# Optimization experiments

Measured on AMD Instinct MI355X. Metric: run time of the kernel, lower is better.

Reference implementation:

```python
import jax, jax.numpy as jnp
import numpy as np

B, T, E, H, V = 64, 160, 512, 1024, 32000


def setup_inputs() -> dict:
    key = jax.random.key(0)
    ks = jax.random.split(key, 8)
    s = 1.0 / np.sqrt(H).astype(np.float32)
    return {
        "contexts": jax.random.randint(ks[0], (B, T), 0, V),
        "responses": jax.random.randint(ks[1], (B, T), 0, V),
        "emb": jax.random.normal(ks[2], (V, E), jnp.float32) * 0.02,
        "Wih": jax.random.uniform(ks[3], (4 * H, E), jnp.float32, -s, s),
        "Whh": jax.random.uniform(ks[4], (4 * H, H), jnp.float32, -s, s),
        "bih": jax.random.uniform(ks[5], (4 * H,), jnp.float32, -s, s),
        "bhh": jax.random.uniform(ks[6], (4 * H,), jnp.float32, -s, s),
        "M": jax.random.normal(ks[7], (H, H), jnp.float32),
    }


def _lstm_final_h(tokens, emb, Wih, Whh, bih, bhh):
    """Single-layer LSTM (PyTorch gate order i,f,g,o); returns final hidden state [B,H]."""
    x = emb[tokens]                      # [B, T, E]
    b = bih + bhh                        # [4H]
    hdim = Whh.shape[1]

    def step(carry, xt):
        h, c = carry
        gates = xt @ Wih.T + h @ Whh.T + b          # [B, 4H]
        i, f, g, o = jnp.split(gates, 4, axis=-1)
        c = jax.nn.sigmoid(f) * c + jax.nn.sigmoid(i) * jnp.tanh(g)
        h = jax.nn.sigmoid(o) * jnp.tanh(c)
        return (h, c), None

    h0 = jnp.zeros((tokens.shape[0], hdim), x.dtype)
    (h, _), _ = jax.lax.scan(step, (h0, h0), jnp.swapaxes(x, 0, 1))  # scan over time
    return h


def reference(contexts, responses, emb, Wih, Whh, bih, bhh, M):
    ch = _lstm_final_h(contexts, emb, Wih, Whh, bih, bhh)   # [B, H]
    rh = _lstm_final_h(responses, emb, Wih, Whh, bih, bhh)  # [B, H]
    # batched bilinear: sigmoid(diag(C @ M @ R^T)) -- replaces the per-example Python loop
    return jax.nn.sigmoid(jnp.einsum('bi,ij,bj->b', ch, M, rh))
```

## Files before the change

kernel.cpp:

```cpp
#include <hip/hip_runtime.h>
#include <math.h>


#define BB 64
#define TT 160
#define EE 512
#define HH 1024
#define G4 4096
#define ROWS 128
#define NBLK 64

typedef unsigned short u16;
typedef unsigned int u32;
typedef __attribute__((ext_vector_type(8))) __bf16 bf16x8;
typedef __attribute__((ext_vector_type(8))) short short8;
typedef __attribute__((ext_vector_type(4))) short short4v;
typedef __attribute__((ext_vector_type(4))) float f32x4;
typedef __attribute__((ext_vector_type(2))) u32 u32x2;

__device__ __forceinline__ u16 f2b(float f) {
    unsigned u = __float_as_uint(f);
    u = u + 0x7fffu + ((u >> 16) & 1u);
    return (u16)(u >> 16);
}
__device__ __forceinline__ float b2f(u16 s) { return __uint_as_float(((unsigned)s) << 16); }

#define LOG2E 1.4426950408889634f
__device__ __forceinline__ float sigf(float x) {
    return __builtin_amdgcn_rcpf(1.f + __builtin_amdgcn_exp2f(-LOG2E * x));
}
__device__ __forceinline__ float tanhf_fast(float x) {
    return 1.f - 2.f * __builtin_amdgcn_rcpf(1.f + __builtin_amdgcn_exp2f(2.f * LOG2E * x));
}

__device__ __forceinline__ f32x4 mfma16(short8 a, short8 b, f32x4 c) {
    return __builtin_amdgcn_mfma_f32_16x16x32_bf16(
        __builtin_bit_cast(bf16x8, a), __builtin_bit_cast(bf16x8, b), c, 0, 0, 0);
}

__device__ __forceinline__ void g2l16(const void* gsrc, void* ldst) {
    __builtin_amdgcn_global_load_lds(
        (const __attribute__((address_space(1))) u32*)gsrc,
        (__attribute__((address_space(3))) u32*)ldst, 16, 0, 0);
}
__device__ __forceinline__ void g2l16c(const void* gsrc, void* ldst) {
    __builtin_amdgcn_global_load_lds(
        (const __attribute__((address_space(1))) u32*)gsrc,
        (__attribute__((address_space(3))) u32*)ldst, 16, 0, 17);
}

__global__ __launch_bounds__(256) void cvt_kernel(const float* __restrict__ in,
                                                  u16* __restrict__ out, int n4) {
    int i = blockIdx.x * 256 + threadIdx.x;
    if (i < n4) {
        f32x4 v = *(const f32x4*)(in + (size_t)i * 4);
        short4v o;
        o.x = (short)f2b(v.x); o.y = (short)f2b(v.y);
        o.z = (short)f2b(v.z); o.w = (short)f2b(v.w);
        *(short4v*)(out + (size_t)i * 4) = o;
    }
}

__global__ __launch_bounds__(256) void pre_gemm2(
    const int* __restrict__ ctx, const int* __restrict__ rsp,
    const u16* __restrict__ embb, const u16* __restrict__ Wihb,
    const float* __restrict__ bih, const float* __restrict__ bhh,
    u16* __restrict__ xg)
{
    __shared__ __align__(16) u16 As[2][128][64];
    __shared__ __align__(16) u16 Ws[2][128][64];
    __shared__ int toks[128];
    const int tid = threadIdx.x;
    const int n0 = blockIdx.x * 128;
    const int t  = blockIdx.y;

    if (tid < 128) {
        int r = tid;
        toks[tid] = (r < BB) ? ctx[r * TT + t] : rsp[(r - BB) * TT + t];
    }
    __syncthreads();

    const u16* asrc[4]; const u16* bsrc[4];
    #pragma unroll
    for (int q = 0; q < 4; ++q) {
        int i = tid + q * 256;
        int row = i >> 3, c16 = i & 7;
        int scol = ((c16 ^ (row & 7)) * 8);
        asrc[q] = embb + (size_t)toks[row] * EE + scol;
        bsrc[q] = Wihb + (size_t)(n0 + row) * EE + scol;
    }

    const int lane = tid & 63, wave = tid >> 6;
    const int wr = (wave >> 1) * 64, wc = (wave & 1) * 64;
    const int l15 = lane & 15, l4 = lane >> 4;
    f32x4 acc[4][4] = {};

    #pragma unroll
    for (int q = 0; q < 4; ++q) {
        g2l16(asrc[q], (char*)&As[0][0][0] + (tid + q * 256) * 16);
        g2l16(bsrc[q], (char*)&Ws[0][0][0] + (tid + q * 256) * 16);
    }
    for (int it = 0; it < 8; ++it) {
        __syncthreads();
        if (it + 1 < 8) {
            int kk = (it + 1) * 64, bs = (it + 1) & 1;
            #pragma unroll
            for (int q = 0; q < 4; ++q) {
                g2l16(asrc[q] + kk, (char*)&As[bs][0][0] + (tid + q * 256) * 16);
                g2l16(bsrc[q] + kk, (char*)&Ws[bs][0][0] + (tid + q * 256) * 16);
            }
        }
        const int b = it & 1;
        #pragma unroll
        for (int ks = 0; ks < 2; ++ks) {
            int c16 = ks * 4 + l4;
            short8 a[4], w[4];
            #pragma unroll
            for (int mf = 0; mf < 4; ++mf) {
                int R = wr + mf * 16 + l15;
                a[mf] = *(const short8*)((const char*)&As[b][0][0] + R * 128 + ((c16 ^ (R & 7)) << 4));
            }
            #pragma unroll
            for (int nf = 0; nf < 4; ++nf) {
                int Nn = wc + nf * 16 + l15;
                w[nf] = *(const short8*)((const char*)&Ws[b][0][0] + Nn * 128 + ((c16 ^ (Nn & 7)) << 4));
            }
            #pragma unroll
            for (int mf = 0; mf < 4; ++mf)
                #pragma unroll
                for (int nf = 0; nf < 4; ++nf)
                    acc[mf][nf] = mfma16(a[mf], w[nf], acc[mf][nf]);
        }
    }

    u16* xp = xg + (size_t)t * ROWS * G4;
    #pragma unroll
    for (int nf = 0; nf < 4; ++nf) {
        int n = n0 + wc + nf * 16 + l15;
        float bias = bih[n] + bhh[n];
        #pragma unroll
        for (int mf = 0; mf < 4; ++mf)
            #pragma unroll
            for (int q = 0; q < 4; ++q) {
                int r = wr + mf * 16 + l4 * 4 + q;
                xp[(size_t)r * G4 + n] = f2b(acc[mf][nf][q] + bias);
            }
    }
}

__global__ __launch_bounds__(512, 2) void lstm_persist7(
    const u16* __restrict__ Whhb, const u16* __restrict__ xg,
    u16* __restrict__ hbuf, u32* __restrict__ barr)
{
    __shared__ __align__(16) u16 Abuf[2][64][512];

    const int tid = threadIdx.x;
    const int bx = blockIdx.x;
    const int cg = bx & 31, rg = bx >> 5;
    const int r0 = rg * 64, j0 = cg * 32;
    const int lane = tid & 63, w = tid >> 6;
    const int colt = w >> 2, q = w & 3;
    const int l15 = lane & 15, l4 = lane >> 4;

    float* const G = (float*)&Abuf[0][0][0];

    short8 breg[4][8];
    #pragma unroll
    for (int nt = 0; nt < 4; ++nt) {
        int n = (colt * 2 + (nt >> 1)) * 1024 + j0 + (nt & 1) * 16 + l15;
        const u16* wp = Whhb + (size_t)n * HH + l4 * 8;
        #pragma unroll
        for (int z = 0; z < 8; ++z) {
            int kc = (z < 4) ? (q * 4 + z) : (16 + q * 4 + (z - 4));
            breg[nt][z] = *(const short8*)(wp + kc * 32);
        }
    }

    const int urow = tid >> 3;
    const int jj4  = (tid & 7) * 4;
    float cst[4] = {0.f, 0.f, 0.f, 0.f};

    u32* const cb = barr + (size_t)rg * 2048;

    __syncthreads();

    for (int t = 0; t < TT; ++t) {
        const u16* hin = hbuf + (size_t)(t & 1) * ROWS * HH;
        u16* hout      = hbuf + (size_t)((t + 1) & 1) * ROWS * HH;

        #pragma unroll
        for (int j = 0; j < 8; ++j) {
            int row = w * 8 + j;
            const u16* src = hin + (size_t)(r0 + row) * HH + ((lane ^ (row & 7)) * 8);
            g2l16c(src,       &Abuf[0][row][0]);
            g2l16c(src + 512, &Abuf[1][row][0]);
        }
        u32x2 xv[4];
        {
            const u16* xp = xg + ((size_t)t * ROWS + r0 + urow) * G4 + j0 + jj4;
            #pragma unroll
            for (int g = 0; g < 4; ++g)
                asm volatile("global_load_dwordx2 %0, %1, off"
                             : "=v"(xv[g]) : "v"(xp + g * HH));
        }

        f32x4 acc[4][4] = {};

        asm volatile("s_waitcnt vmcnt(4)" ::: "memory");
        __builtin_amdgcn_sched_barrier(0);
        __builtin_amdgcn_s_barrier();
        __builtin_amdgcn_sched_barrier(0);
        #pragma unroll
        for (int half = 0; half < 2; ++half) {
            #pragma unroll
            for (int z4 = 0; z4 < 4; ++z4) {
                const int kcl = q * 4 + z4;
                short8 a[4];
                #pragma unroll
                for (int rt = 0; rt < 4; ++rt) {
                    int row = rt * 16 + l15;
                    int c16 = kcl * 4 + l4;
                    a[rt] = *(const short8*)((const char*)&Abuf[half][0][0] +
                             row * 1024 + ((c16 ^ (l15 & 7)) << 4));
                }
                #pragma unroll
                for (int rt = 0; rt < 4; ++rt)
                    #pragma unroll
                    for (int nt = 0; nt < 4; ++nt)
                        acc[rt][nt] = mfma16(a[rt], breg[nt][half * 4 + z4], acc[rt][nt]);
            }
        }
        asm volatile("s_waitcnt lgkmcnt(0)" ::: "memory");
        __builtin_amdgcn_s_barrier();
        __builtin_amdgcn_sched_barrier(0);

        if (q < 2) {
            #pragma unroll
            for (int rt = 0; rt < 4; ++rt)
                #pragma unroll
                for (int nt = 0; nt < 4; ++nt) {
                    int col = colt * 64 + nt * 16 + l15;
                    int rowb = rt * 16 + l4 * 4;
                    #pragma unroll
                    for (int e = 0; e < 4; ++e)
                        G[((size_t)q * 64 + rowb + e) * 132 + col] = acc[rt][nt][e];
                }
        }
        asm volatile("s_waitcnt lgkmcnt(0)" ::: "memory");
        __builtin_amdgcn_s_barrier();
        __builtin_amdgcn_sched_barrier(0);
        if (q >= 2) {
            #pragma unroll
            for (int rt = 0; rt < 4; ++rt)
                #pragma unroll
                for (int nt = 0; nt < 4; ++nt) {
                    int col = colt * 64 + nt * 16 + l15;
                    int rowb = rt * 16 + l4 * 4;
                    #pragma unroll
                    for (int e = 0; e < 4; ++e)
                        G[((size_t)(q - 2) * 64 + rowb + e) * 132 + col] += acc[rt][nt][e];
                }
        }
        asm volatile("s_waitcnt lgkmcnt(0)" ::: "memory");
        __builtin_amdgcn_s_barrier();
        __builtin_amdgcn_sched_barrier(0);

        asm volatile("s_waitcnt vmcnt(0)" ::: "memory");
        float gv[4][4];
        #pragma unroll
        for (int g = 0; g < 4; ++g) {
            const float* Gr0 = &G[((size_t)0 * 64 + urow) * 132 + g * 32 + jj4];
            const float* Gr1 = &G[((size_t)1 * 64 + urow) * 132 + g * 32 + jj4];
            f32x4 a0 = *(const f32x4*)Gr0;
            f32x4 a1 = *(const f32x4*)Gr1;
            gv[g][0] = a0.x + a1.x + b2f((u16)(xv[g].x & 0xffffu));
            gv[g][1] = a0.y + a1.y + b2f((u16)(xv[g].x >> 16));
            gv[g][2] = a0.z + a1.z + b2f((u16)(xv[g].y & 0xffffu));
            gv[g][3] = a0.w + a1.w + b2f((u16)(xv[g].y >> 16));
        }
        u16 hp[4];
        #pragma unroll
        for (int e = 0; e < 4; ++e) {
            float ii = sigf(gv[0][e]);
            float ff = sigf(gv[1][e]);
            float gg = tanhf_fast(gv[2][e]);
            float oo = sigf(gv[3][e]);
            cst[e] = ff * cst[e] + ii * gg;
            hp[e] = f2b(oo * tanhf_fast(cst[e]));
        }
        u32x2 hw;
        hw.x = (u32)hp[0] | ((u32)hp[1] << 16);
        hw.y = (u32)hp[2] | ((u32)hp[3] << 16);
        {
            u16* hpt = hout + (size_t)(r0 + urow) * HH + j0 + jj4;
            asm volatile("global_store_dwordx2 %0, %1, off sc0 sc1"
                         :: "v"(hpt), "v"(hw) : "memory");
        }

        if (t < TT - 1) {
            asm volatile("s_waitcnt vmcnt(0)" ::: "memory");
            __builtin_amdgcn_s_barrier();
            __builtin_amdgcn_sched_barrier(0);
            const u32 target = (u32)(t + 1);
            if (tid == 0)
                asm volatile("global_store_dword %0, %1, off sc0 sc1"
                             :: "v"(cb + cg * 32), "v"(target) : "memory");
            if (w == 0) {
                const u32* fp = cb + (lane & 31) * 32;
                int spins = 0;
                while (true) {
                    u32 v;
                    asm volatile("global_load_dword %0, %1, off sc0 sc1"
                                 : "=v"(v) : "v"(fp));
                    asm volatile("s_waitcnt vmcnt(0)" ::: "memory");
                    if (__all(v >= target)) break;
                    __builtin_amdgcn_s_sleep(1);
                    if (++spins > 2000000) break;
                }
            }
            __builtin_amdgcn_s_barrier();
            __builtin_amdgcn_sched_barrier(0);
        }
    }
}

template<int MODE>
__global__ __launch_bounds__(256) void step_fused(
    const int* __restrict__ ctx, const int* __restrict__ rsp,
    const u16* __restrict__ embb, const u16* __restrict__ Wihb,
    const u16* __restrict__ Whhb, const u16* __restrict__ xg,
    const float* __restrict__ bih, const float* __restrict__ bhh,
    const u16* __restrict__ hin, u16* __restrict__ hout,
    float* __restrict__ c_ws, int t)
{
    __shared__ __align__(16) u16 As[2][64][64];
    __shared__ __align__(16) u16 Ws[2][32][64];
    __shared__ float gs[64][32];
    __shared__ int toks[64];

    const int tid = threadIdx.x;
    const int cg = blockIdx.x & 127, rg = blockIdx.x >> 7;
    const int r0 = rg * 64, j0 = cg * 8;

    if (MODE == 1) {
        if (tid < 64) {
            int r = r0 + tid;
            toks[tid] = (r < BB) ? ctx[r * TT + t] : rsp[(r - BB) * TT + t];
        }
        __syncthreads();
    }

    const int arow0 = tid >> 3, c16a = tid & 7;
    const int arow1 = arow0 + 32;
    const int acol0 = ((c16a ^ (arow0 & 7)) * 8);
    const int acol1 = ((c16a ^ (arow1 & 7)) * 8);
    const u16* hA0 = hin + (size_t)(r0 + arow0) * HH + acol0;
    const u16* hA1 = hin + (size_t)(r0 + arow1) * HH + acol1;
    const u16* eA0 = nullptr; const u16* eA1 = nullptr;
    if (MODE == 1) {
        eA0 = embb + (size_t)toks[arow0] * EE + acol0;
        eA1 = embb + (size_t)toks[arow1] * EE + acol1;
    }
    const int nn = tid >> 3, c16b = tid & 7;
    const int bcol = ((c16b ^ (nn & 7)) * 8);
    const int wrow = (nn >> 3) * HH + j0 + (nn & 7);
    const u16* wHh = Whhb + (size_t)wrow * HH + bcol;
    const u16* wIh = (MODE == 1) ? (Wihb + (size_t)wrow * EE + bcol) : nullptr;

    const int NK = (MODE == 1) ? 24 : 16;

    auto stage = [&](int bs, int it) {
        int kk = it * 64;
        const u16 *s0, *s1, *sw;
        if (MODE == 1 && kk < EE) {
            s0 = eA0 + kk; s1 = eA1 + kk; sw = wIh + kk;
        } else {
            int khh = (MODE == 1) ? kk - EE : kk;
            s0 = hA0 + khh; s1 = hA1 + khh; sw = wHh + khh;
        }
        g2l16(s0, (char*)&As[bs][0][0] + tid * 16);
        g2l16(s1, (char*)&As[bs][0][0] + (tid + 256) * 16);
        g2l16(sw, (char*)&Ws[bs][0][0] + tid * 16);
    };

    const int lane = tid & 63, wave = tid >> 6;
    const int wr = wave * 16;
    const int l15 = lane & 15, l4 = lane >> 4;
    f32x4 acc[2] = {};

    stage(0, 0);
    for (int it = 0; it < NK; ++it) {
        __syncthreads();
        if (it + 1 < NK) stage((it + 1) & 1, it + 1);
        const int b = it & 1;
        #pragma unroll
        for (int ks = 0; ks < 2; ++ks) {
            int c16 = ks * 4 + l4;
            int R = wr + l15;
            short8 a = *(const short8*)((const char*)&As[b][0][0] + R * 128 + ((c16 ^ (R & 7)) << 4));
            #pragma unroll
            for (int nf = 0; nf < 2; ++nf) {
                int Nn = nf * 16 + l15;
                short8 w = *(const short8*)((const char*)&Ws[b][0][0] + Nn * 128 + ((c16 ^ (Nn & 7)) << 4));
                acc[nf] = mfma16(a, w, acc[nf]);
            }
        }
    }
    __syncthreads();
    #pragma unroll
    for (int nf = 0; nf < 2; ++nf)
        #pragma unroll
        for (int q = 0; q < 4; ++q)
            gs[wr + l4 * 4 + q][nf * 16 + l15] = acc[nf][q];
    __syncthreads();

    const int e = tid * 2;
    const int row = e >> 3, jj = e & 7;
    const int rglob = r0 + row;
    float g0[4], g1[4];
    #pragma unroll
    for (int g = 0; g < 4; ++g) { g0[g] = gs[row][g * 8 + jj]; g1[g] = gs[row][g * 8 + jj + 1]; }
    if (MODE == 2) {
        const u16* xp = xg + ((size_t)t * ROWS + rglob) * G4 + j0 + jj;
        #pragma unroll
        for (int g = 0; g < 4; ++g) { g0[g] += b2f(xp[g * HH]); g1[g] += b2f(xp[g * HH + 1]); }
    } else {
        #pragma unroll
        for (int g = 0; g < 4; ++g) {
            int n = g * HH + j0 + jj;
            g0[g] += bih[n] + bhh[n];
            g1[g] += bih[n + 1] + bhh[n + 1];
        }
    }
    size_t cidx = ((size_t)blockIdx.x * 64 + row) * 8 + jj;
    float c0 = c_ws[cidx], c1 = c_ws[cidx + 1];
    float i0 = 1.f / (1.f + expf(-g0[0])), i1 = 1.f / (1.f + expf(-g1[0]));
    float f0 = 1.f / (1.f + expf(-g0[1])), f1 = 1.f / (1.f + expf(-g1[1]));
    float t0 = tanhf(g0[2]),               t1 = tanhf(g1[2]);
    float o0 = 1.f / (1.f + expf(-g0[3])), o1 = 1.f / (1.f + expf(-g1[3]));
    float cn0 = f0 * c0 + i0 * t0;
    float cn1 = f1 * c1 + i1 * t1;
    c_ws[cidx] = cn0; c_ws[cidx + 1] = cn1;
    float h0 = o0 * tanhf(cn0), h1 = o1 * tanhf(cn1);
    unsigned hpk = (unsigned)f2b(h0) | ((unsigned)f2b(h1) << 16);
    *(unsigned*)(hout + (size_t)rglob * HH + j0 + jj) = hpk;
}

__global__ __launch_bounds__(256) void step_gemm_f32(
    const int* __restrict__ ctx, const int* __restrict__ rsp,
    const float* __restrict__ emb, const float* __restrict__ Wih, const float* __restrict__ Whh,
    const u16* __restrict__ hb, float* __restrict__ gates, int t)
{
    __shared__ __align__(16) u16 As[64][32];
    __shared__ __align__(16) u16 Ws[64][32];
    __shared__ int toks[64];
    const int tid = threadIdx.x;
    const int n0 = blockIdx.x * 64;
    const int r0 = blockIdx.y * 64;
    const int part = blockIdx.z;
    if (tid < 64) {
        int r = r0 + tid;
        toks[tid] = (r < BB) ? ctx[r * TT + t] : rsp[(r - BB) * TT + t];
    }
    __syncthreads();
    const int lane = tid & 63, wave = tid >> 6;
    const int wr = (wave >> 1) * 32, wc = (wave & 1) * 32;
    const int l15 = lane & 15, l4 = lane >> 4;
    f32x4 acc[2][2] = {};
    const int kstart = part * 768;
    const int srow = tid >> 2;
    const int sseg = (tid & 3) * 8;
    for (int it = 0; it < 24; ++it) {
        const int kg = kstart + it * 32;
        const int kk = kg + sseg;
        if (kg < EE) {
            const float* s = emb + (size_t)toks[srow] * EE + kk;
            #pragma unroll
            for (int q = 0; q < 8; ++q) As[srow][sseg + q] = f2b(s[q]);
            const float* sw = Wih + (size_t)(n0 + srow) * EE + kk;
            #pragma unroll
            for (int q = 0; q < 8; ++q) Ws[srow][sseg + q] = f2b(sw[q]);
        } else {
            *(short8*)&As[srow][sseg] = *(const short8*)(hb + (size_t)(r0 + srow) * HH + (kk - EE));
            const float* sw = Whh + (size_t)(n0 + srow) * HH + (kk - EE);
            #pragma unroll
            for (int q = 0; q < 8; ++q) Ws[srow][sseg + q] = f2b(sw[q]);
        }
        __syncthreads();
        #pragma unroll
        for (int mf = 0; mf < 2; ++mf)
            #pragma unroll
            for (int nf = 0; nf < 2; ++nf)
                acc[mf][nf] = mfma16(*(const short8*)&As[wr + mf * 16 + l15][l4 * 8],
                                     *(const short8*)&Ws[wc + nf * 16 + l15][l4 * 8], acc[mf][nf]);
        __syncthreads();
    }
    float* gp = gates + (size_t)part * ROWS * G4;
    #pragma unroll
    for (int mf = 0; mf < 2; ++mf)
        #pragma unroll
        for (int nf = 0; nf < 2; ++nf)
            #pragma unroll
            for (int q = 0; q < 4; ++q) {
                int r = r0 + wr + mf * 16 + l4 * 4 + q;
                int n = n0 + wc + nf * 16 + l15;
                gp[(size_t)r * G4 + n] = acc[mf][nf][q];
            }
}

__global__ __launch_bounds__(256) void lstm_update0(
    const float* __restrict__ gates, const float* __restrict__ bih, const float* __restrict__ bhh,
    u16* __restrict__ hb, float* __restrict__ c)
{
    int idx = blockIdx.x * 256 + threadIdx.x;
    int r = idx >> 8;
    int jj = (idx & 255) * 4;
    const float* gp0 = gates + (size_t)r * G4;
    const float* gp1 = gates + (size_t)(ROWS + r) * G4;
    float gate[4][4];
    #pragma unroll
    for (int g = 0; g < 4; ++g) {
        int n = g * HH + jj;
        f32x4 a = *(const f32x4*)(gp0 + n);
        f32x4 b = *(const f32x4*)(gp1 + n);
        #pragma unroll
        for (int q = 0; q < 4; ++q) gate[g][q] = a[q] + b[q] + bih[n + q] + bhh[n + q];
    }
    int cidx = r * HH + jj;
    f32x4 cv = *(const f32x4*)(c + cidx);
    f32x4 cn; short4v hn;
    #pragma unroll
    for (int q = 0; q < 4; ++q) {
        float si = 1.f / (1.f + expf(-gate[0][q]));
        float sf = 1.f / (1.f + expf(-gate[1][q]));
        float tg = tanhf(gate[2][q]);
        float so = 1.f / (1.f + expf(-gate[3][q]));
        float cval = sf * cv[q] + si * tg;
        cn[q] = cval;
        ((short*)&hn)[q] = (short)f2b(so * tanhf(cval));
    }
    *(f32x4*)(c + cidx) = cn;
    *(short4v*)(hb + cidx) = hn;
}

__global__ __launch_bounds__(256) void bilinear(
    const u16* __restrict__ hb, const float* __restrict__ M, float* __restrict__ out)
{
    int b = blockIdx.x;
    __shared__ float chs[HH];
    __shared__ float red[256];
    const u16* ch = hb + (size_t)b * HH;
    const u16* rh = hb + (size_t)(BB + b) * HH;
    for (int i = threadIdx.x; i < HH; i += 256) chs[i] = b2f(ch[i]);
    __syncthreads();
    float vj[4] = {0.f, 0.f, 0.f, 0.f};
    for (int i = 0; i < HH; ++i) {
        float chi = chs[i];
        const float* Mr = M + (size_t)i * HH;
        #pragma unroll
        for (int q = 0; q < 4; ++q) vj[q] += chi * Mr[threadIdx.x + q * 256];
    }
    float acc = 0.f;
    #pragma unroll
    for (int q = 0; q < 4; ++q) acc += vj[q] * b2f(rh[threadIdx.x + q * 256]);
    red[threadIdx.x] = acc;
    __syncthreads();
    for (int s = 128; s > 0; s >>= 1) {
        if (threadIdx.x < s) red[threadIdx.x] += red[threadIdx.x + s];
        __syncthreads();
    }
    if (threadIdx.x == 0) out[b] = 1.0f / (1.0f + expf(-red[0]));
}

extern "C" void kernel_launch(void* const* d_in, const int* in_sizes, int n_in,
                              void* d_out, int out_size, void* d_ws, size_t ws_size,
                              hipStream_t stream) {
    const int*   ctx = (const int*)d_in[0];
    const int*   rsp = (const int*)d_in[1];
    const float* emb = (const float*)d_in[2];
    const float* Wih = (const float*)d_in[3];
    const float* Whh = (const float*)d_in[4];
    const float* bih = (const float*)d_in[5];
    const float* bhh = (const float*)d_in[6];
    const float* M   = (const float*)d_in[7];
    float* out = (float*)d_out;

    char* w = (char*)d_ws;
    u16*   hbuf  = (u16*)w;   w += (size_t)2 * ROWS * HH * 2;
    float* c_ws  = (float*)w; w += (size_t)ROWS * HH * 4;
    float* gates = (float*)w; w += (size_t)2 * ROWS * G4 * 4;
    u16*   embb  = (u16*)w;   w += (size_t)32000 * EE * 2;
    u16*   Wihb  = (u16*)w;   w += (size_t)G4 * EE * 2;
    u16*   Whhb  = (u16*)w;   w += (size_t)G4 * HH * 2;
    u32*   barr  = (u32*)w;   w += 16384;
    size_t conv_need = (size_t)(w - (char*)d_ws);
    u16*   xg    = (u16*)w;   w += (size_t)TT * ROWS * G4 * 2;
    size_t xpre_need = (size_t)(w - (char*)d_ws);

    int mode = (ws_size >= xpre_need) ? 2 : (ws_size >= conv_need) ? 1 : 0;

    hipMemsetAsync(hbuf, 0, (size_t)2 * ROWS * HH * 2, stream);

    if (mode >= 1) {
        cvt_kernel<<<16000, 256, 0, stream>>>(emb, embb, 32000 * EE / 4);
        cvt_kernel<<<2048,  256, 0, stream>>>(Wih, Wihb, G4 * EE / 4);
        cvt_kernel<<<4096,  256, 0, stream>>>(Whh, Whhb, G4 * HH / 4);
    }

    if (mode == 2) {
        hipMemsetAsync(barr, 0, 16384, stream);
        pre_gemm2<<<dim3(G4 / 128, TT), 256, 0, stream>>>(ctx, rsp, embb, Wihb, bih, bhh, xg);
        lstm_persist7<<<NBLK, 512, 0, stream>>>(Whhb, xg, hbuf, barr);
        bilinear<<<BB, 256, 0, stream>>>(hbuf, M, out);
    } else if (mode == 1) {
        hipMemsetAsync(c_ws, 0, (size_t)ROWS * HH * 4, stream);
        for (int t = 0; t < TT; ++t) {
            const u16* hin = hbuf + (size_t)(t & 1) * ROWS * HH;
            u16* hout      = hbuf + (size_t)((t + 1) & 1) * ROWS * HH;
            step_fused<1><<<256, 256, 0, stream>>>(ctx, rsp, embb, Wihb, Whhb, xg,
                                                   bih, bhh, hin, hout, c_ws, t);
        }
        bilinear<<<BB, 256, 0, stream>>>(hbuf, M, out);
    } else {
        hipMemsetAsync(c_ws, 0, (size_t)ROWS * HH * 4, stream);
        u16* hb = hbuf;
        dim3 sg(G4 / 64, ROWS / 64, 2);
        for (int t = 0; t < TT; ++t) {
            step_gemm_f32<<<sg, 256, 0, stream>>>(ctx, rsp, emb, Wih, Whh, hb, gates, t);
            lstm_update0<<<128, 256, 0, stream>>>(gates, bih, bhh, hb, c_ws);
        }
        bilinear<<<BB, 256, 0, stream>>>(hb, M, out);
    }
}
```

Before: 1.899 ms.

## Replace persistent LSTM kernel with per-timestep launches using stream ordering

Drops the persistent kernel that synchronised blocks through a global-memory spin barrier and instead launches one kernel per timestep, with the cell state kept in a global workspace. The aim is to remove the cost and fragility of the software grid barrier and its polling. In exchange every step pays launch overhead and must reload the recurrent weight slice into registers and read/write the cell state from global memory.

```diff
diff --git a/kernel.cpp b/kernel.cpp
--- a/kernel.cpp
+++ b/kernel.cpp
@@ -42,11 +42,6 @@
     __builtin_amdgcn_global_load_lds(
         (const __attribute__((address_space(1))) u32*)gsrc,
         (__attribute__((address_space(3))) u32*)ldst, 16, 0, 0);
-}
-__device__ __forceinline__ void g2l16c(const void* gsrc, void* ldst) {
-    __builtin_amdgcn_global_load_lds(
-        (const __attribute__((address_space(1))) u32*)gsrc,
-        (__attribute__((address_space(3))) u32*)ldst, 16, 0, 17);
 }
 
 __global__ __launch_bounds__(256) void cvt_kernel(const float* __restrict__ in,
@@ -148,9 +143,10 @@
     }
 }
 
-__global__ __launch_bounds__(512, 2) void lstm_persist7(
+__global__ __launch_bounds__(512) void lstm_step(
     const u16* __restrict__ Whhb, const u16* __restrict__ xg,
-    u16* __restrict__ hbuf, u32* __restrict__ barr)
+    const u16* __restrict__ hin, u16* __restrict__ hout,
+    float* __restrict__ c_ws, int t)
 {
     __shared__ __align__(16) u16 Abuf[2][64][512];
 
@@ -164,6 +160,14 @@
 
     float* const G = (float*)&Abuf[0][0][0];
 
+    #pragma unroll
+    for (int j = 0; j < 8; ++j) {
+        int row = w * 8 + j;
+        const u16* src = hin + (size_t)(r0 + row) * HH + ((lane ^ (row & 7)) * 8);
+        g2l16(src,       &Abuf[0][row][0]);
+        g2l16(src + 512, &Abuf[1][row][0]);
+    }
+
     short8 breg[4][8];
     #pragma unroll
     for (int nt = 0; nt < 4; ++nt) {
@@ -178,150 +182,94 @@
 
     const int urow = tid >> 3;
     const int jj4  = (tid & 7) * 4;
-    float cst[4] = {0.f, 0.f, 0.f, 0.f};
-
-    u32* const cb = barr + (size_t)rg * 2048;
-
-    __syncthreads();
-
-    for (int t = 0; t < TT; ++t) {
-        const u16* hin = hbuf + (size_t)(t & 1) * ROWS * HH;
-        u16* hout      = hbuf + (size_t)((t + 1) & 1) * ROWS * HH;
-
-        #pragma unroll
-        for (int j = 0; j < 8; ++j) {
-            int row = w * 8 + j;
-            const u16* src = hin + (size_t)(r0 + row) * HH + ((lane ^ (row & 7)) * 8);
-            g2l16c(src,       &Abuf[0][row][0]);
-            g2l16c(src + 512, &Abuf[1][row][0]);
-        }
-        u32x2 xv[4];
-        {
-            const u16* xp = xg + ((size_t)t * ROWS + r0 + urow) * G4 + j0 + jj4;
-            #pragma unroll
-            for (int g = 0; g < 4; ++g)
-                asm volatile("global_load_dwordx2 %0, %1, off"
-                             : "=v"(xv[g]) : "v"(xp + g * HH));
-        }
-
-        f32x4 acc[4][4] = {};
-
-        asm volatile("s_waitcnt vmcnt(4)" ::: "memory");
-        __builtin_amdgcn_sched_barrier(0);
-        __builtin_amdgcn_s_barrier();
-        __builtin_amdgcn_sched_barrier(0);
-        #pragma unroll
-        for (int half = 0; half < 2; ++half) {
-            #pragma unroll
-            for (int z4 = 0; z4 < 4; ++z4) {
-                const int kcl = q * 4 + z4;
-                short8 a[4];
-                #pragma unroll
-                for (int rt = 0; rt < 4; ++rt) {
-                    int row = rt * 16 + l15;
-                    int c16 = kcl * 4 + l4;
-                    a[rt] = *(const short8*)((const char*)&Abuf[half][0][0] +
-                             row * 1024 + ((c16 ^ (l15 & 7)) << 4));
-                }
-                #pragma unroll
-                for (int rt = 0; rt < 4; ++rt)
-                    #pragma unroll
-                    for (int nt = 0; nt < 4; ++nt)
-                        acc[rt][nt] = mfma16(a[rt], breg[nt][half * 4 + z4], acc[rt][nt]);
-            }
-        }
-        asm volatile("s_waitcnt lgkmcnt(0)" ::: "memory");
-        __builtin_amdgcn_s_barrier();
-        __builtin_amdgcn_sched_barrier(0);
-
-        if (q < 2) {
+    u32x2 xv[4];
+    {
+        const u16* xp = xg + ((size_t)t * ROWS + r0 + urow) * G4 + j0 + jj4;
+        #pragma unroll
+        for (int g = 0; g < 4; ++g) xv[g] = *(const u32x2*)(xp + g * HH);
+    }
+    const size_t cidx = ((size_t)bx * 512 + tid) * 4;
+    f32x4 cv = *(const f32x4*)(c_ws + cidx);
+
+    __syncthreads();
+
+    f32x4 acc[4][4] = {};
+    #pragma unroll
+    for (int half = 0; half < 2; ++half) {
+        #pragma unroll
+        for (int z4 = 0; z4 < 4; ++z4) {
+            const int kcl = q * 4 + z4;
+            short8 a[4];
+            #pragma unroll
+            for (int rt = 0; rt < 4; ++rt) {
+                int row = rt * 16 + l15;
+                int c16 = kcl * 4 + l4;
+                a[rt] = *(const short8*)((const char*)&Abuf[half][0][0] +
+                         row * 1024 + ((c16 ^ (l15 & 7)) << 4));
+            }
             #pragma unroll
             for (int rt = 0; rt < 4; ++rt)
                 #pragma unroll
-                for (int nt = 0; nt < 4; ++nt) {
-                    int col = colt * 64 + nt * 16 + l15;
-                    int rowb = rt * 16 + l4 * 4;
-                    #pragma unroll
-                    for (int e = 0; e < 4; ++e)
-                        G[((size_t)q * 64 + rowb + e) * 132 + col] = acc[rt][nt][e];
-                }
-        }
-        asm volatile("s_waitcnt lgkmcnt(0)" ::: "memory");
-        __builtin_amdgcn_s_barrier();
-        __builtin_amdgcn_sched_barrier(0);
-        if (q >= 2) {
-            #pragma unroll
-            for (int rt = 0; rt < 4; ++rt)
+                for (int nt = 0; nt < 4; ++nt)
+                    acc[rt][nt] = mfma16(a[rt], breg[nt][half * 4 + z4], acc[rt][nt]);
+        }
+    }
+    __syncthreads();
+
+    if (q < 2) {
+        #pragma unroll
+        for (int rt = 0; rt < 4; ++rt)
+            #pragma unroll
+            for (int nt = 0; nt < 4; ++nt) {
+                int col = colt * 64 + nt * 16 + l15;
+                int rowb = rt * 16 + l4 * 4;
                 #pragma unroll
-                for (int nt = 0; nt < 4; ++nt) {
-                    int col = colt * 64 + nt * 16 + l15;
-                    int rowb = rt * 16 + l4 * 4;
-                    #pragma unroll
-                    for (int e = 0; e < 4; ++e)
-                        G[((size_t)(q - 2) * 64 + rowb + e) * 132 + col] += acc[rt][nt][e];
-                }
-        }
-        asm volatile("s_waitcnt lgkmcnt(0)" ::: "memory");
-        __builtin_amdgcn_s_barrier();
-        __builtin_amdgcn_sched_barrier(0);
-
-        asm volatile("s_waitcnt vmcnt(0)" ::: "memory");
-        float gv[4][4];
-        #pragma unroll
-        for (int g = 0; g < 4; ++g) {
-            const float* Gr0 = &G[((size_t)0 * 64 + urow) * 132 + g * 32 + jj4];
-            const float* Gr1 = &G[((size_t)1 * 64 + urow) * 132 + g * 32 + jj4];
-            f32x4 a0 = *(const f32x4*)Gr0;
-            f32x4 a1 = *(const f32x4*)Gr1;
-            gv[g][0] = a0.x + a1.x + b2f((u16)(xv[g].x & 0xffffu));
-            gv[g][1] = a0.y + a1.y + b2f((u16)(xv[g].x >> 16));
-            gv[g][2] = a0.z + a1.z + b2f((u16)(xv[g].y & 0xffffu));
-            gv[g][3] = a0.w + a1.w + b2f((u16)(xv[g].y >> 16));
-        }
-        u16 hp[4];
-        #pragma unroll
-        for (int e = 0; e < 4; ++e) {
-            float ii = sigf(gv[0][e]);
-            float ff = sigf(gv[1][e]);
-            float gg = tanhf_fast(gv[2][e]);
-            float oo = sigf(gv[3][e]);
-            cst[e] = ff * cst[e] + ii * gg;
-            hp[e] = f2b(oo * tanhf_fast(cst[e]));
-        }
-        u32x2 hw;
-        hw.x = (u32)hp[0] | ((u32)hp[1] << 16);
-        hw.y = (u32)hp[2] | ((u32)hp[3] << 16);
-        {
-            u16* hpt = hout + (size_t)(r0 + urow) * HH + j0 + jj4;
-            asm volatile("global_store_dwordx2 %0, %1, off sc0 sc1"
-                         :: "v"(hpt), "v"(hw) : "memory");
-        }
-
-        if (t < TT - 1) {
-            asm volatile("s_waitcnt vmcnt(0)" ::: "memory");
-            __builtin_amdgcn_s_barrier();
-            __builtin_amdgcn_sched_barrier(0);
-            const u32 target = (u32)(t + 1);
-            if (tid == 0)
-                asm volatile("global_store_dword %0, %1, off sc0 sc1"
-                             :: "v"(cb + cg * 32), "v"(target) : "memory");
-            if (w == 0) {
-                const u32* fp = cb + (lane & 31) * 32;
-                int spins = 0;
-                while (true) {
-                    u32 v;
-                    asm volatile("global_load_dword %0, %1, off sc0 sc1"
-                                 : "=v"(v) : "v"(fp));
-                    asm volatile("s_waitcnt vmcnt(0)" ::: "memory");
-                    if (__all(v >= target)) break;
-                    __builtin_amdgcn_s_sleep(1);
-                    if (++spins > 2000000) break;
-                }
-            }
-            __builtin_amdgcn_s_barrier();
-            __builtin_amdgcn_sched_barrier(0);
-        }
-    }
+                for (int e = 0; e < 4; ++e)
+                    G[((size_t)q * 64 + rowb + e) * 132 + col] = acc[rt][nt][e];
+            }
+    }
+    __syncthreads();
+    if (q >= 2) {
+        #pragma unroll
+        for (int rt = 0; rt < 4; ++rt)
+            #pragma unroll
+            for (int nt = 0; nt < 4; ++nt) {
+                int col = colt * 64 + nt * 16 + l15;
+                int rowb = rt * 16 + l4 * 4;
+                #pragma unroll
+                for (int e = 0; e < 4; ++e)
+                    G[((size_t)(q - 2) * 64 + rowb + e) * 132 + col] += acc[rt][nt][e];
+            }
+    }
+    __syncthreads();
+
+    float gv[4][4];
+    #pragma unroll
+    for (int g = 0; g < 4; ++g) {
+        f32x4 a0 = *(const f32x4*)&G[((size_t)0 * 64 + urow) * 132 + g * 32 + jj4];
+        f32x4 a1 = *(const f32x4*)&G[((size_t)1 * 64 + urow) * 132 + g * 32 + jj4];
+        gv[g][0] = a0.x + a1.x + b2f((u16)(xv[g].x & 0xffffu));
+        gv[g][1] = a0.y + a1.y + b2f((u16)(xv[g].x >> 16));
+        gv[g][2] = a0.z + a1.z + b2f((u16)(xv[g].y & 0xffffu));
+        gv[g][3] = a0.w + a1.w + b2f((u16)(xv[g].y >> 16));
+    }
+    f32x4 cn;
+    u16 hp[4];
+    #pragma unroll
+    for (int e = 0; e < 4; ++e) {
+        float ii = sigf(gv[0][e]);
+        float ff = sigf(gv[1][e]);
+        float gg = tanhf_fast(gv[2][e]);
+        float oo = sigf(gv[3][e]);
+        float cval = ff * cv[e] + ii * gg;
+        cn[e] = cval;
+        hp[e] = f2b(oo * tanhf_fast(cval));
+    }
+    *(f32x4*)(c_ws + cidx) = cn;
+    u32x2 hw;
+    hw.x = (u32)hp[0] | ((u32)hp[1] << 16);
+    hw.y = (u32)hp[2] | ((u32)hp[3] << 16);
+    *(u32x2*)(hout + (size_t)(r0 + urow) * HH + j0 + jj4) = hw;
 }
 
 template<int MODE>
@@ -592,7 +540,6 @@
     u16*   embb  = (u16*)w;   w += (size_t)32000 * EE * 2;
     u16*   Wihb  = (u16*)w;   w += (size_t)G4 * EE * 2;
     u16*   Whhb  = (u16*)w;   w += (size_t)G4 * HH * 2;
-    u32*   barr  = (u32*)w;   w += 16384;
     size_t conv_need = (size_t)(w - (char*)d_ws);
     u16*   xg    = (u16*)w;   w += (size_t)TT * ROWS * G4 * 2;
     size_t xpre_need = (size_t)(w - (char*)d_ws);
@@ -600,6 +547,7 @@
     int mode = (ws_size >= xpre_need) ? 2 : (ws_size >= conv_need) ? 1 : 0;
 
     hipMemsetAsync(hbuf, 0, (size_t)2 * ROWS * HH * 2, stream);
+    hipMemsetAsync(c_ws, 0, (size_t)ROWS * HH * 4, stream);
 
     if (mode >= 1) {
         cvt_kernel<<<16000, 256, 0, stream>>>(emb, embb, 32000 * EE / 4);
@@ -608,12 +556,14 @@
     }
 
     if (mode == 2) {
-        hipMemsetAsync(barr, 0, 16384, stream);
         pre_gemm2<<<dim3(G4 / 128, TT), 256, 0, stream>>>(ctx, rsp, embb, Wihb, bih, bhh, xg);
-        lstm_persist7<<<NBLK, 512, 0, stream>>>(Whhb, xg, hbuf, barr);
+        for (int t = 0; t < TT; ++t) {
+            const u16* hin = hbuf + (size_t)(t & 1) * ROWS * HH;
+            u16* hout      = hbuf + (size_t)((t + 1) & 1) * ROWS * HH;
+            lstm_step<<<NBLK, 512, 0, stream>>>(Whhb, xg, hin, hout, c_ws, t);
+        }
         bilinear<<<BB, 256, 0, stream>>>(hbuf, M, out);
     } else if (mode == 1) {
-        hipMemsetAsync(c_ws, 0, (size_t)ROWS * HH * 4, stream);
         for (int t = 0; t < TT; ++t) {
             const u16* hin = hbuf + (size_t)(t & 1) * ROWS * HH;
             u16* hout      = hbuf + (size_t)((t + 1) & 1) * ROWS * HH;
@@ -622,7 +572,6 @@
         }
         bilinear<<<BB, 256, 0, stream>>>(hbuf, M, out);
     } else {
-        hipMemsetAsync(c_ws, 0, (size_t)ROWS * HH * 4, stream);
         u16* hb = hbuf;
         dim3 sg(G4 / 64, ROWS / 64, 2);
         for (int t = 0; t < TT; ++t) {
```

Result: slower. 2.530 ms (+33.2%).

## Replace global barrier with per-wave flag waits and direct global h loads

Applied to the files above, without the earlier changes.

The persistent LSTM kernel drops its block-wide all-to-all spin barrier. Each wave now waits only on the flags of the column groups whose hidden-state slices it reads, then loads h straight from global memory into registers with a software-pipelined loop. The LDS staging buffer for h is removed, leaving LDS only for the gate-reduction scratch. This aims to cut synchronization latency on each timestep, at the cost of more global load traffic and more fine-grained flag polling. The c_ws memset is also moved so it runs in every mode.

```diff
diff --git a/kernel.cpp b/kernel.cpp
--- a/kernel.cpp
+++ b/kernel.cpp
@@ -42,11 +42,6 @@
     __builtin_amdgcn_global_load_lds(
         (const __attribute__((address_space(1))) u32*)gsrc,
         (__attribute__((address_space(3))) u32*)ldst, 16, 0, 0);
-}
-__device__ __forceinline__ void g2l16c(const void* gsrc, void* ldst) {
-    __builtin_amdgcn_global_load_lds(
-        (const __attribute__((address_space(1))) u32*)gsrc,
-        (__attribute__((address_space(3))) u32*)ldst, 16, 0, 17);
 }
 
 __global__ __launch_bounds__(256) void cvt_kernel(const float* __restrict__ in,
@@ -148,11 +143,11 @@
     }
 }
 
-__global__ __launch_bounds__(512, 2) void lstm_persist7(
+__global__ __launch_bounds__(512) void lstm_persist9(
     const u16* __restrict__ Whhb, const u16* __restrict__ xg,
     u16* __restrict__ hbuf, u32* __restrict__ barr)
 {
-    __shared__ __align__(16) u16 Abuf[2][64][512];
+    __shared__ __align__(16) float G[2][64][132];
 
     const int tid = threadIdx.x;
     const int bx = blockIdx.x;
@@ -162,8 +157,6 @@
     const int colt = w >> 2, q = w & 3;
     const int l15 = lane & 15, l4 = lane >> 4;
 
-    float* const G = (float*)&Abuf[0][0][0];
-
     short8 breg[4][8];
     #pragma unroll
     for (int nt = 0; nt < 4; ++nt) {
@@ -181,6 +174,8 @@
     float cst[4] = {0.f, 0.f, 0.f, 0.f};
 
     u32* const cb = barr + (size_t)rg * 2048;
+    const u32* const myflags = cb + (size_t)(((lane & 7) < 4 ? (q * 4 + (lane & 7))
+                                            : (16 + q * 4 + ((lane & 7) - 4)))) * 32;
 
     __syncthreads();
 
@@ -188,13 +183,6 @@
         const u16* hin = hbuf + (size_t)(t & 1) * ROWS * HH;
         u16* hout      = hbuf + (size_t)((t + 1) & 1) * ROWS * HH;
 
-        #pragma unroll
-        for (int j = 0; j < 8; ++j) {
-            int row = w * 8 + j;
-            const u16* src = hin + (size_t)(r0 + row) * HH + ((lane ^ (row & 7)) * 8);
-            g2l16c(src,       &Abuf[0][row][0]);
-            g2l16c(src + 512, &Abuf[1][row][0]);
-        }
         u32x2 xv[4];
         {
             const u16* xp = xg + ((size_t)t * ROWS + r0 + urow) * G4 + j0 + jj4;
@@ -204,35 +192,51 @@
                              : "=v"(xv[g]) : "v"(xp + g * HH));
         }
 
+        if (t > 0) {
+            const u32 tgt = (u32)t;
+            int spins = 0;
+            while (true) {
+                u32 v;
+                asm volatile("global_load_dword %0, %1, off sc0 sc1"
+                             : "=v"(v) : "v"(myflags));
+                asm volatile("s_waitcnt vmcnt(0)" ::: "memory");
+                if (__all(v >= tgt)) break;
+                __builtin_amdgcn_s_sleep(2);
+                if (++spins > 4000000) break;
+            }
+            __builtin_amdgcn_sched_barrier(0);
+        }
+
         f32x4 acc[4][4] = {};
-
-        asm volatile("s_waitcnt vmcnt(4)" ::: "memory");
-        __builtin_amdgcn_sched_barrier(0);
-        __builtin_amdgcn_s_barrier();
-        __builtin_amdgcn_sched_barrier(0);
-        #pragma unroll
-        for (int half = 0; half < 2; ++half) {
-            #pragma unroll
-            for (int z4 = 0; z4 < 4; ++z4) {
-                const int kcl = q * 4 + z4;
-                short8 a[4];
-                #pragma unroll
-                for (int rt = 0; rt < 4; ++rt) {
-                    int row = rt * 16 + l15;
-                    int c16 = kcl * 4 + l4;
-                    a[rt] = *(const short8*)((const char*)&Abuf[half][0][0] +
-                             row * 1024 + ((c16 ^ (l15 & 7)) << 4));
-                }
+        short8 acur[4], anxt[4];
+        #pragma unroll
+        for (int z = 0; z < 8; ++z) {
+            const int p = (z < 4) ? (q * 4 + z) : (16 + q * 4 + (z - 4));
+            #pragma unroll
+            for (int rt = 0; rt < 4; ++rt) {
+                const u16* src = hin + (size_t)(r0 + rt * 16 + l15) * HH + p * 32 + l4 * 8;
+                asm volatile("global_load_dwordx4 %0, %1, off sc0 sc1"
+                             : "=v"(anxt[rt]) : "v"(src));
+            }
+            if (z > 0) {
+                asm volatile("s_waitcnt vmcnt(4)" ::: "memory");
+                __builtin_amdgcn_sched_barrier(0);
                 #pragma unroll
                 for (int rt = 0; rt < 4; ++rt)
                     #pragma unroll
                     for (int nt = 0; nt < 4; ++nt)
-                        acc[rt][nt] = mfma16(a[rt], breg[nt][half * 4 + z4], acc[rt][nt]);
-            }
-        }
-        asm volatile("s_waitcnt lgkmcnt(0)" ::: "memory");
-        __builtin_amdgcn_s_barrier();
+                        acc[rt][nt] = mfma16(acur[rt], breg[nt][z - 1], acc[rt][nt]);
+            }
+            #pragma unroll
+            for (int rt = 0; rt < 4; ++rt) acur[rt] = anxt[rt];
+        }
+        asm volatile("s_waitcnt vmcnt(0)" ::: "memory");
         __builtin_amdgcn_sched_barrier(0);
+        #pragma unroll
+        for (int rt = 0; rt < 4; ++rt)
+            #pragma unroll
+            for (int nt = 0; nt < 4; ++nt)
+                acc[rt][nt] = mfma16(acur[rt], breg[nt][7], acc[rt][nt]);
 
         if (q < 2) {
             #pragma unroll
@@ -243,7 +247,7 @@
                     int rowb = rt * 16 + l4 * 4;
                     #pragma unroll
                     for (int e = 0; e < 4; ++e)
-                        G[((size_t)q * 64 + rowb + e) * 132 + col] = acc[rt][nt][e];
+                        G[q][rowb + e][col] = acc[rt][nt][e];
                 }
         }
         asm volatile("s_waitcnt lgkmcnt(0)" ::: "memory");
@@ -258,21 +262,18 @@
                     int rowb = rt * 16 + l4 * 4;
                     #pragma unroll
                     for (int e = 0; e < 4; ++e)
-                        G[((size_t)(q - 2) * 64 + rowb + e) * 132 + col] += acc[rt][nt][e];
+                        G[q - 2][rowb + e][col] += acc[rt][nt][e];
                 }
         }
         asm volatile("s_waitcnt lgkmcnt(0)" ::: "memory");
         __builtin_amdgcn_s_barrier();
         __builtin_amdgcn_sched_barrier(0);
 
-        asm volatile("s_waitcnt vmcnt(0)" ::: "memory");
         float gv[4][4];
         #pragma unroll
         for (int g = 0; g < 4; ++g) {
-            const float* Gr0 = &G[((size_t)0 * 64 + urow) * 132 + g * 32 + jj4];
-            const float* Gr1 = &G[((size_t)1 * 64 + urow) * 132 + g * 32 + jj4];
-            f32x4 a0 = *(const f32x4*)Gr0;
-            f32x4 a1 = *(const f32x4*)Gr1;
+            f32x4 a0 = *(const f32x4*)&G[0][urow][g * 32 + jj4];
+            f32x4 a1 = *(const f32x4*)&G[1][urow][g * 32 + jj4];
             gv[g][0] = a0.x + a1.x + b2f((u16)(xv[g].x & 0xffffu));
             gv[g][1] = a0.y + a1.y + b2f((u16)(xv[g].x >> 16));
             gv[g][2] = a0.z + a1.z + b2f((u16)(xv[g].y & 0xffffu));
@@ -301,25 +302,11 @@
             asm volatile("s_waitcnt vmcnt(0)" ::: "memory");
             __builtin_amdgcn_s_barrier();
             __builtin_amdgcn_sched_barrier(0);
-            const u32 target = (u32)(t + 1);
-            if (tid == 0)
+            if (tid == 0) {
+                const u32 val = (u32)(t + 1);
                 asm volatile("global_store_dword %0, %1, off sc0 sc1"
-                             :: "v"(cb + cg * 32), "v"(target) : "memory");
-            if (w == 0) {
-                const u32* fp = cb + (lane & 31) * 32;
-                int spins = 0;
-                while (true) {
-                    u32 v;
-                    asm volatile("global_load_dword %0, %1, off sc0 sc1"
-                                 : "=v"(v) : "v"(fp));
-                    asm volatile("s_waitcnt vmcnt(0)" ::: "memory");
-                    if (__all(v >= target)) break;
-                    __builtin_amdgcn_s_sleep(1);
-                    if (++spins > 2000000) break;
-                }
-            }
-            __builtin_amdgcn_s_barrier();
-            __builtin_amdgcn_sched_barrier(0);
+                             :: "v"(cb + cg * 32), "v"(val) : "memory");
+            }
         }
     }
 }
@@ -600,6 +587,7 @@
     int mode = (ws_size >= xpre_need) ? 2 : (ws_size >= conv_need) ? 1 : 0;
 
     hipMemsetAsync(hbuf, 0, (size_t)2 * ROWS * HH * 2, stream);
+    hipMemsetAsync(c_ws, 0, (size_t)ROWS * HH * 4, stream);
 
     if (mode >= 1) {
         cvt_kernel<<<16000, 256, 0, stream>>>(emb, embb, 32000 * EE / 4);
@@ -610,10 +598,9 @@
     if (mode == 2) {
         hipMemsetAsync(barr, 0, 16384, stream);
         pre_gemm2<<<dim3(G4 / 128, TT), 256, 0, stream>>>(ctx, rsp, embb, Wihb, bih, bhh, xg);
-        lstm_persist7<<<NBLK, 512, 0, stream>>>(Whhb, xg, hbuf, barr);
+        lstm_persist9<<<NBLK, 512, 0, stream>>>(Whhb, xg, hbuf, barr);
         bilinear<<<BB, 256, 0, stream>>>(hbuf, M, out);
     } else if (mode == 1) {
-        hipMemsetAsync(c_ws, 0, (size_t)ROWS * HH * 4, stream);
         for (int t = 0; t < TT; ++t) {
             const u16* hin = hbuf + (size_t)(t & 1) * ROWS * HH;
             u16* hout      = hbuf + (size_t)((t + 1) & 1) * ROWS * HH;
@@ -622,7 +609,6 @@
         }
         bilinear<<<BB, 256, 0, stream>>>(hbuf, M, out);
     } else {
-        hipMemsetAsync(c_ws, 0, (size_t)ROWS * HH * 4, stream);
         u16* hb = hbuf;
         dim3 sg(G4 / 64, ROWS / 64, 2);
         for (int t = 0; t < TT; ++t) {
```

Result: slower. 2.169 ms (+14.2%).
